# Kernel optimization log

Measured on AMD Instinct MI355X. Metric: run time of the kernel, lower is better.

The kernel has to match this reference:

```python
import jax, jax.numpy as jnp
import numpy as np

N0, N1, N2 = 100000, 20000, 4000   # nodes per hierarchy level
F, H, C = 128, 128, 10             # num_features, hidden_dim, num_classes
E0, E1, E2 = 1600000, 320000, 64000  # intra-level edges (avg degree 16)
EPS = 1e-5                          # BatchNorm eps


def setup_inputs() -> dict:
    key = jax.random.key(0)
    ks = jax.random.split(key, 16)
    s = 0.05
    return {
        "x": jax.random.normal(ks[0], (N0, F), jnp.float32),
        "ei0": jax.random.randint(ks[1], (2, E0), 0, N0),
        "ei1": jax.random.randint(ks[2], (2, E1), 0, N1),
        "ei2": jax.random.randint(ks[3], (2, E2), 0, N2),
        "parent1": jax.random.randint(ks[4], (N0,), 0, N1),
        "parent2": jax.random.randint(ks[5], (N1,), 0, N2),
        "W0": jax.random.normal(ks[6], (F, H), jnp.float32) * s,
        "b0": jnp.zeros((H,), jnp.float32),
        "W1": jax.random.normal(ks[7], (H, H), jnp.float32) * s,
        "b1": jnp.zeros((H,), jnp.float32),
        "W2": jax.random.normal(ks[8], (H, H), jnp.float32) * s,
        "b2": jnp.zeros((H,), jnp.float32),
        "W3": jax.random.normal(ks[9], (2 * H, H), jnp.float32) * s,
        "b3": jnp.zeros((H,), jnp.float32),
        "W4": jax.random.normal(ks[10], (2 * H, C), jnp.float32) * s,
        "b4": jnp.zeros((C,), jnp.float32),
        "pW": jax.random.normal(ks[11], (4, H, H), jnp.float32) * s,
        "pb": jnp.zeros((4, H), jnp.float32),
        "pgamma": jnp.ones((4, H), jnp.float32),
        "pbeta": jnp.zeros((4, H), jnp.float32),
        "pmean": jax.random.normal(ks[12], (4, H), jnp.float32) * 0.1,
        "pvar": jax.random.uniform(ks[13], (4, H), jnp.float32, 0.5, 1.5),
    }


def _gcn(x, ei, W, b):
    # GCNConv: add self loops, symmetric D^-1/2 (A+I) D^-1/2 normalization.
    n = x.shape[0]
    loops = jnp.arange(n)
    row = jnp.concatenate([ei[0], loops])  # source nodes
    col = jnp.concatenate([ei[1], loops])  # target nodes
    deg = jax.ops.segment_sum(jnp.ones(row.shape, x.dtype), col, num_segments=n)
    dis = deg ** -0.5  # deg >= 1 because of self loops
    norm = dis[row] * dis[col]
    xw = x @ W
    out = jax.ops.segment_sum(norm[:, None] * xw[row], col, num_segments=n)
    return out + b


def _pool_nn(y, W, b, g, beta, mean, var):
    # SEPooling nn: Linear -> ReLU -> BatchNorm1d (eval mode, running stats)
    y = jax.nn.relu(y @ W + b)
    return (y - mean) * (g / jnp.sqrt(var + EPS)) + beta


def reference(x, ei0, ei1, ei2, parent1, parent2,
              W0, b0, W1, b1, W2, b2, W3, b3, W4, b4,
              pW, pb, pgamma, pbeta, pmean, pvar):
    relu = jax.nn.relu
    # down path (dropout is identity in eval mode)
    h0 = relu(_gcn(x, ei0, W0, b0))  # [N0,H]; stored skip xs[0]
    p = jax.ops.segment_sum(h0, parent1, num_segments=N1)  # scatter-add children -> parents
    x1 = relu(_pool_nn(p, pW[0], pb[0], pgamma[0], pbeta[0], pmean[0], pvar[0]))
    h1 = relu(_gcn(x1, ei1, W1, b1))  # [N1,H]; stored skip xs[1]
    p = jax.ops.segment_sum(h1, parent2, num_segments=N2)
    x2 = relu(_pool_nn(p, pW[1], pb[1], pgamma[1], pbeta[1], pmean[1], pvar[1]))
    # up path: conv, unpool (gather parent feature per child), concat skip
    h = relu(_gcn(x2, ei2, W2, b2))  # [N2,H]
    xu = relu(_pool_nn(h[parent2], pW[2], pb[2], pgamma[2], pbeta[2], pmean[2], pvar[2]))  # [N1,H]
    xc = jnp.concatenate([xu, h1], axis=1)  # [N1,2H]
    h = relu(_gcn(xc, ei1, W3, b3))  # [N1,H]
    xu = relu(_pool_nn(h[parent1], pW[3], pb[3], pgamma[3], pbeta[3], pmean[3], pvar[3]))  # [N0,H]
    xc = jnp.concatenate([xu, h0], axis=1)  # [N0,2H]
    out = _gcn(xc, ei0, W4, b4)  # [N0,C]
    return jax.nn.log_softmax(out, axis=-1)
```

## Files before the change

kernel.cpp:

```cpp
#include <hip/hip_runtime.h>
#include <math.h>

#define N0 100000
#define N1 20000
#define N2 4000
#define HDIM 128
#define E0C 1600000
#define E1C 320000
#define E2C 64000
#define EPSBN 1e-5f

typedef unsigned int u32;
typedef float f32x4 __attribute__((ext_vector_type(4)));
typedef short bf16x8 __attribute__((ext_vector_type(8)));

union FragU { uint4 u; bf16x8 h; };
__device__ __forceinline__ bf16x8 asbf(uint4 v) { FragU x; x.u = v; return x.h; }

__device__ __forceinline__ float bl(u32 p) { return __uint_as_float(p << 16); }
__device__ __forceinline__ float bh(u32 p) { return __uint_as_float(p & 0xFFFF0000u); }
__device__ __forceinline__ u32 pack2(float a, float b) {
    u32 ua = __float_as_uint(a), ub = __float_as_uint(b);
    ua = (ua + 0x7FFFu + ((ua >> 16) & 1u)) >> 16;
    ub = (ub + 0x7FFFu + ((ub >> 16) & 1u)) >> 16;
    return ua | (ub << 16);
}

#define OFF0 0
#define OFF1 (N0)
#define OFF2 (N0 + N1)
#define OFF3 (N0 + N1 + N2)
#define OFF4 (N0 + N1 + N2 + N1)
#define OFFT (N0 + N1 + N2 + N1 + N2)

#define S0 (E0C)
#define S1 (E0C + E1C)
#define S2 (E0C + E1C + E2C)
#define S3 (E0C + E1C + E2C + N0)
#define S4 (E0C + E1C + E2C + N0 + N1)

#define NBUCK ((OFFT + 1023) / 1024)
#define ITEMS_PER_BLK 2048
#define NBA ((S4 + ITEMS_PER_BLK - 1) / ITEMS_PER_BLK)
#define BH_N (NBUCK * NBA)
#define NBLK2 ((BH_N + 1023) / 1024)

#define NWMAT 9


__device__ __forceinline__ void item_full(int g,
    const int* __restrict__ ei0r, const int* __restrict__ ei0c,
    const int* __restrict__ ei1r, const int* __restrict__ ei1c,
    const int* __restrict__ ei2r, const int* __restrict__ ei2c,
    const int* __restrict__ p1, const int* __restrict__ p2,
    int& concat, int& payload)
{
    if (g < S0)      { concat = ei0c[g];             payload = ei0r[g]; }
    else if (g < S1) { int i = g - S0; concat = OFF1 + ei1c[i]; payload = ei1r[i]; }
    else if (g < S2) { int i = g - S1; concat = OFF2 + ei2c[i]; payload = ei2r[i]; }
    else if (g < S3) { int i = g - S2; concat = OFF3 + p1[i];   payload = i; }
    else             { int i = g - S3; concat = OFF4 + p2[i];   payload = i; }
}

__device__ __forceinline__ int item_concat(int g,
    const int* __restrict__ ei0c, const int* __restrict__ ei1c, const int* __restrict__ ei2c,
    const int* __restrict__ p1, const int* __restrict__ p2)
{
    if (g < S0)      return ei0c[g];
    else if (g < S1) return OFF1 + ei1c[g - S0];
    else if (g < S2) return OFF2 + ei2c[g - S1];
    else if (g < S3) return OFF3 + p1[g - S2];
    else             return OFF4 + p2[g - S3];
}

__global__ __launch_bounds__(256) void binhist_kernel(
    const int* __restrict__ ei0c, const int* __restrict__ ei1c, const int* __restrict__ ei2c,
    const int* __restrict__ p1, const int* __restrict__ p2,
    int* __restrict__ blockHist,
    const float* __restrict__ W0p, const float* __restrict__ W1p,
    const float* __restrict__ W2p, const float* __restrict__ W3p,
    const float* __restrict__ pWp, u32* __restrict__ Wpk)
{
    __shared__ int hist[NBUCK];
    int tid = threadIdx.x, blk = blockIdx.x;
    if (blk >= NBA) {
        int b = blk - NBA;
        const float* src;
        if (b == 0) src = W0p;
        else if (b == 1) src = W1p;
        else if (b == 2) src = W2p;
        else if (b == 3) src = W3p;
        else if (b == 4) src = W3p + 128 * 128;
        else src = pWp + (b - 5) * 128 * 128;
        u32* dst = Wpk + b * 8192;
        #pragma unroll
        for (int it = 0; it < 32; it++) {
            int flat = it * 256 + tid;
            int i = flat & 3;
            int ln = (flat >> 2) & 63;
            int s = (flat >> 8) & 3;
            int t = flat >> 10;
            int mm = ln & 15, qq = ln >> 4;
            int k0 = s * 32 + qq * 8 + 2 * i;
            int col = t * 16 + mm;
            dst[flat] = pack2(src[k0 * 128 + col], src[(k0 + 1) * 128 + col]);
        }
        return;
    }
    for (int i = tid; i < NBUCK; i += 256) hist[i] = 0;
    __syncthreads();
    int base = blk * ITEMS_PER_BLK;
    #pragma unroll
    for (int k = 0; k < ITEMS_PER_BLK / 256; k++) {
        int g = base + k * 256 + tid;
        if (g < S4) {
            int c = item_concat(g, ei0c, ei1c, ei2c, p1, p2);
            atomicAdd(&hist[c >> 10], 1);
        }
    }
    __syncthreads();
    for (int b = tid; b < NBUCK; b += 256) blockHist[b * NBA + blk] = hist[b];
}

__global__ __launch_bounds__(256) void scan_k1(const int* __restrict__ c, int* __restrict__ bsum, int n) {
    int t = threadIdx.x;
    int base = blockIdx.x * 1024 + t * 4;
    int s = 0;
    #pragma unroll
    for (int j = 0; j < 4; j++) {
        int idx = base + j;
        if (idx < n) s += c[idx];
    }
    #pragma unroll
    for (int o = 32; o > 0; o >>= 1) s += __shfl_down(s, o, 64);
    __shared__ int ws[4];
    if ((t & 63) == 0) ws[t >> 6] = s;
    __syncthreads();
    if (t == 0) bsum[blockIdx.x] = ws[0] + ws[1] + ws[2] + ws[3];
}

__global__ __launch_bounds__(256) void scan_k2(int* __restrict__ bsum, int* __restrict__ totalOut, int nb,
    const float* __restrict__ g, const float* __restrict__ beta,
    const float* __restrict__ mean, const float* __restrict__ var,
    float* __restrict__ scale, float* __restrict__ shift)
{
    int t = threadIdx.x;
    #pragma unroll
    for (int j = 0; j < 2; j++) {
        int i = j * 256 + t;
        float s = g[i] * rsqrtf(var[i] + EPSBN);
        scale[i] = s;
        shift[i] = beta[i] - mean[i] * s;
    }
    int v = (t < nb) ? bsum[t] : 0;
    __shared__ int ts[256];
    ts[t] = v;
    __syncthreads();
    for (int o = 1; o < 256; o <<= 1) {
        int u = (t >= o) ? ts[t - o] : 0;
        __syncthreads();
        ts[t] += u;
        __syncthreads();
    }
    if (t < nb) bsum[t] = ts[t] - v;
    if (t == nb - 1) *totalOut = ts[t];
}

__global__ __launch_bounds__(256) void scan_k3(const int* __restrict__ c, const int* __restrict__ bsum,
                                               const int* __restrict__ total,
                                               int* __restrict__ S, int n) {
    int t = threadIdx.x;
    int base = blockIdx.x * 1024 + t * 4;
    int v[4];
    #pragma unroll
    for (int j = 0; j < 4; j++) v[j] = (base + j < n) ? c[base + j] : 0;
    int tsum = v[0] + v[1] + v[2] + v[3];
    __shared__ int ts[256];
    ts[t] = tsum;
    __syncthreads();
    for (int o = 1; o < 256; o <<= 1) {
        int u = (t >= o) ? ts[t - o] : 0;
        __syncthreads();
        ts[t] += u;
        __syncthreads();
    }
    int run = bsum[blockIdx.x] + ts[t] - tsum;
    #pragma unroll
    for (int j = 0; j < 4; j++) {
        if (base + j < n) { S[base + j] = run; run += v[j]; }
    }
    if (blockIdx.x == 0 && t == 0) S[n] = *total;
}

__global__ __launch_bounds__(256) void binfill_kernel(
    const int* __restrict__ ei0r, const int* __restrict__ ei0c,
    const int* __restrict__ ei1r, const int* __restrict__ ei1c,
    const int* __restrict__ ei2r, const int* __restrict__ ei2c,
    const int* __restrict__ p1, const int* __restrict__ p2,
    const int* __restrict__ OfsAbs, u32* __restrict__ binPair)
{
    __shared__ int cur[NBUCK];
    int tid = threadIdx.x, blk = blockIdx.x;
    for (int i = tid; i < NBUCK; i += 256) cur[i] = OfsAbs[i * NBA + blk];
    __syncthreads();
    int base = blk * ITEMS_PER_BLK;
    #pragma unroll
    for (int k = 0; k < ITEMS_PER_BLK / 256; k++) {
        int g = base + k * 256 + tid;
        if (g < S4) {
            int c, p;
            item_full(g, ei0r, ei0c, ei1r, ei1c, ei2r, ei2c, p1, p2, c, p);
            int pos = atomicAdd(&cur[c >> 10], 1);
            binPair[pos] = ((u32)(c & 1023) << 17) | (u32)p;
        }
    }
}

__global__ __launch_bounds__(1024) void bucket_build_kernel(
    const u32* __restrict__ binPair, const int* __restrict__ OfsAbs,
    int* __restrict__ rpAll, int* __restrict__ srcU,
    float* __restrict__ dis0, float* __restrict__ dis1, float* __restrict__ dis2)
{
    __shared__ int cnt_l[1024];
    __shared__ int rp_l[1024];
    __shared__ int ts2[1024];
    int b = blockIdx.x, tid = threadIdx.x;
    int start = OfsAbs[b * NBA];
    int end = (b + 1 < NBUCK) ? OfsAbs[(b + 1) * NBA] : S4;
    int d0 = b << 10;
    int nd = OFFT - d0; if (nd > 1024) nd = 1024;

    cnt_l[tid] = 0;
    __syncthreads();
    for (int i = start + tid; i < end; i += 1024) {
        u32 e = binPair[i];
        atomicAdd(&cnt_l[e >> 17], 1);
    }
    __syncthreads();
    int v = cnt_l[tid];
    ts2[tid] = v;
    __syncthreads();
    for (int o = 1; o < 1024; o <<= 1) {
        int u = (tid >= o) ? ts2[tid - o] : 0;
        __syncthreads();
        ts2[tid] += u;
        __syncthreads();
    }
    rp_l[tid] = ts2[tid] - v;
    __syncthreads();
    if (tid < nd) {
        int g = d0 + tid;
        rpAll[g] = start + rp_l[tid];
        float dv = rsqrtf((float)(v + 1));
        if (g < OFF1) dis0[g] = dv;
        else if (g < OFF2) dis1[g - OFF1] = dv;
        else if (g < OFF3) dis2[g - OFF2] = dv;
    }
    if (b == NBUCK - 1 && tid == 0) rpAll[OFFT] = S4;
    __syncthreads();
    for (int i = start + tid; i < end; i += 1024) {
        u32 e = binPair[i];
        int pos = start + atomicAdd(&rp_l[e >> 17], 1);
        srcU[pos] = (int)(e & 0x1FFFFu);
    }
}


#define G128_LOAD(sym, off) u32 sym = y[(long long)srcl[e + off] * 64 + lane]

__global__ __launch_bounds__(256) void gather128_kernel(
    const int* __restrict__ rp, const int* __restrict__ srcl,
    const u32* __restrict__ y, const float* __restrict__ dis,
    const float* __restrict__ bias, u32* __restrict__ h, int n)
{
    int wid = (int)((blockIdx.x * 256 + threadIdx.x) >> 6);
    int lane = threadIdx.x & 63;
    if (wid >= n) return;
    u32 self = y[(long long)wid * 64 + lane];
    float ax = bl(self), ay = bh(self);
    int e = rp[wid], e1 = rp[wid + 1];
    for (; e + 7 < e1; e += 8) {
        G128_LOAD(p0, 0); G128_LOAD(p1, 1); G128_LOAD(p2, 2); G128_LOAD(p3, 3);
        G128_LOAD(p4, 4); G128_LOAD(p5, 5); G128_LOAD(p6, 6); G128_LOAD(p7, 7);
        ax += ((bl(p0) + bl(p1)) + (bl(p2) + bl(p3))) + ((bl(p4) + bl(p5)) + (bl(p6) + bl(p7)));
        ay += ((bh(p0) + bh(p1)) + (bh(p2) + bh(p3))) + ((bh(p4) + bh(p5)) + (bh(p6) + bh(p7)));
    }
    if (e + 3 < e1) {
        G128_LOAD(p0, 0); G128_LOAD(p1, 1); G128_LOAD(p2, 2); G128_LOAD(p3, 3);
        ax += (bl(p0) + bl(p1)) + (bl(p2) + bl(p3));
        ay += (bh(p0) + bh(p1)) + (bh(p2) + bh(p3));
        e += 4;
    }
    if (e + 1 < e1) {
        G128_LOAD(p0, 0); G128_LOAD(p1, 1);
        ax += bl(p0) + bl(p1);
        ay += bh(p0) + bh(p1);
        e += 2;
    }
    if (e < e1) {
        G128_LOAD(p0, 0);
        ax += bl(p0); ay += bh(p0);
    }
    float d = dis[wid];
    float2 b = ((const float2*)bias)[lane];
    float r0 = fmaxf(fmaf(d, ax, b.x), 0.f);
    float r1 = fmaxf(fmaf(d, ay, b.y), 0.f);
    h[(long long)wid * 64 + lane] = pack2(r0, r1);
}

__global__ __launch_bounds__(256) void gather10_lsm_kernel(
    const int* __restrict__ rp, const int* __restrict__ srcl,
    const u32* __restrict__ y4, const float* __restrict__ dis,
    const float* __restrict__ bias, float* __restrict__ out, int n)
{
    int c = blockIdx.x * blockDim.x + threadIdx.x;
    if (c >= n) return;
    float acc[10];
    {
        long long base = (long long)c * 8;
        uint4 q = *(const uint4*)(y4 + base);
        u32 q4 = y4[base + 4];
        acc[0] = bl(q.x); acc[1] = bh(q.x);
        acc[2] = bl(q.y); acc[3] = bh(q.y);
        acc[4] = bl(q.z); acc[5] = bh(q.z);
        acc[6] = bl(q.w); acc[7] = bh(q.w);
        acc[8] = bl(q4);  acc[9] = bh(q4);
    }
    int e = rp[c], e1 = rp[c + 1];
    for (; e + 3 < e1; e += 4) {
        long long bA = (long long)srcl[e] * 8;
        long long bB = (long long)srcl[e + 1] * 8;
        long long bC = (long long)srcl[e + 2] * 8;
        long long bD = (long long)srcl[e + 3] * 8;
        uint4 qa = *(const uint4*)(y4 + bA); u32 qa4 = y4[bA + 4];
        uint4 qb = *(const uint4*)(y4 + bB); u32 qb4 = y4[bB + 4];
        uint4 qc = *(const uint4*)(y4 + bC); u32 qc4 = y4[bC + 4];
        uint4 qd = *(const uint4*)(y4 + bD); u32 qd4 = y4[bD + 4];
        acc[0] += (bl(qa.x) + bl(qb.x)) + (bl(qc.x) + bl(qd.x));
        acc[1] += (bh(qa.x) + bh(qb.x)) + (bh(qc.x) + bh(qd.x));
        acc[2] += (bl(qa.y) + bl(qb.y)) + (bl(qc.y) + bl(qd.y));
        acc[3] += (bh(qa.y) + bh(qb.y)) + (bh(qc.y) + bh(qd.y));
        acc[4] += (bl(qa.z) + bl(qb.z)) + (bl(qc.z) + bl(qd.z));
        acc[5] += (bh(qa.z) + bh(qb.z)) + (bh(qc.z) + bh(qd.z));
        acc[6] += (bl(qa.w) + bl(qb.w)) + (bl(qc.w) + bl(qd.w));
        acc[7] += (bh(qa.w) + bh(qb.w)) + (bh(qc.w) + bh(qd.w));
        acc[8] += (bl(qa4) + bl(qb4)) + (bl(qc4) + bl(qd4));
        acc[9] += (bh(qa4) + bh(qb4)) + (bh(qc4) + bh(qd4));
    }
    for (; e < e1; e++) {
        long long bA = (long long)srcl[e] * 8;
        uint4 qa = *(const uint4*)(y4 + bA);
        u32 qa4 = y4[bA + 4];
        acc[0] += bl(qa.x); acc[1] += bh(qa.x);
        acc[2] += bl(qa.y); acc[3] += bh(qa.y);
        acc[4] += bl(qa.z); acc[5] += bh(qa.z);
        acc[6] += bl(qa.w); acc[7] += bh(qa.w);
        acc[8] += bl(qa4);  acc[9] += bh(qa4);
    }
    float d = dis[c];
    float m = -1e30f;
    #pragma unroll
    for (int k = 0; k < 10; k++) {
        acc[k] = fmaf(d, acc[k], bias[k]);
        m = fmaxf(m, acc[k]);
    }
    float s = 0.f;
    #pragma unroll
    for (int k = 0; k < 10; k++) s += expf(acc[k] - m);
    float ls = logf(s);
    #pragma unroll
    for (int k = 0; k < 10; k++) out[(long long)c * 10 + k] = acc[k] - m - ls;
}

__global__ __launch_bounds__(256) void mm128_kernel(
    const void* __restrict__ Av, const u32* __restrict__ Wp,
    u32* __restrict__ out, int M,
    const float* __restrict__ dis,
    const u32* __restrict__ gsrc, const int* __restrict__ gidx,
    const float* __restrict__ bias,
    const float* __restrict__ bnscale, const float* __restrict__ bnshift,
    int pool, int afp32,
    const int* __restrict__ pp, const int* __restrict__ childl, int apool)
{
    __shared__ u32 WL[8192];
    int tid = threadIdx.x;
    {
        const uint4* ws4 = (const uint4*)Wp;
        uint4* wd4 = (uint4*)WL;
        #pragma unroll
        for (int it = 0; it < 8; it++) wd4[it * 256 + tid] = ws4[it * 256 + tid];
    }
    __syncthreads();

    int lane = tid & 63;
    int w = tid >> 6;
    int m = lane & 15, q = lane >> 4;
    int row = blockIdx.x * 64 + w * 16 + m;
    bool live = (row < M);

    uint4 xb[4];
    if (live) {
        if (apool) {
            float fa[32];
            #pragma unroll
            for (int i = 0; i < 32; i++) fa[i] = 0.f;
            const u32* Hb = (const u32*)Av;
            int e = pp[row], eE = pp[row + 1];
            for (; e < eE; e++) {
                long long cb = (long long)childl[e] * 64;
                #pragma unroll
                for (int s = 0; s < 4; s++) {
                    uint4 vv = *(const uint4*)(Hb + cb + s * 16 + q * 4);
                    fa[s * 8 + 0] += bl(vv.x); fa[s * 8 + 1] += bh(vv.x);
                    fa[s * 8 + 2] += bl(vv.y); fa[s * 8 + 3] += bh(vv.y);
                    fa[s * 8 + 4] += bl(vv.z); fa[s * 8 + 5] += bh(vv.z);
                    fa[s * 8 + 6] += bl(vv.w); fa[s * 8 + 7] += bh(vv.w);
                }
            }
            #pragma unroll
            for (int s = 0; s < 4; s++) {
                xb[s].x = pack2(fa[s * 8 + 0], fa[s * 8 + 1]);
                xb[s].y = pack2(fa[s * 8 + 2], fa[s * 8 + 3]);
                xb[s].z = pack2(fa[s * 8 + 4], fa[s * 8 + 5]);
                xb[s].w = pack2(fa[s * 8 + 6], fa[s * 8 + 7]);
            }
        } else if (afp32) {
            const float* Af = (const float*)Av;
            #pragma unroll
            for (int s = 0; s < 4; s++) {
                const float4* p = (const float4*)(Af + (long long)row * 128 + s * 32 + q * 8);
                float4 f0 = p[0], f1 = p[1];
                xb[s].x = pack2(f0.x, f0.y);
                xb[s].y = pack2(f0.z, f0.w);
                xb[s].z = pack2(f1.x, f1.y);
                xb[s].w = pack2(f1.z, f1.w);
            }
        } else {
            const u32* Ab = (const u32*)Av;
            #pragma unroll
            for (int s = 0; s < 4; s++)
                xb[s] = *(const uint4*)(Ab + (long long)row * 64 + s * 16 + q * 4);
        }
    } else {
        xb[0] = xb[1] = xb[2] = xb[3] = make_uint4(0u, 0u, 0u, 0u);
    }

    float d = 1.0f;
    if (dis && live) d = dis[row];
    long long gbase = (gsrc && live) ? (long long)gidx[row] * 64 : 0;

    #pragma unroll
    for (int t = 0; t < 8; t++) {
        f32x4 acc = {0.f, 0.f, 0.f, 0.f};
        #pragma unroll
        for (int s = 0; s < 4; s++) {
            uint4 wa = *(const uint4*)&WL[((t * 4 + s) * 64 + lane) * 4];
            acc = __builtin_amdgcn_mfma_f32_16x16x32_bf16(asbf(wa), asbf(xb[s]), acc, 0, 0, 0);
        }
        if (live) {
            float v0 = acc[0], v1 = acc[1], v2 = acc[2], v3 = acc[3];
            int cbase = t * 16 + q * 4;
            if (gsrc) {
                uint2 g = *(const uint2*)(gsrc + gbase + (cbase >> 1));
                v0 += bl(g.x); v1 += bh(g.x);
                v2 += bl(g.y); v3 += bh(g.y);
            }
            if (pool) {
                float4 bb = *(const float4*)(bias + cbase);
                float4 sc = *(const float4*)(bnscale + cbase);
                float4 sh = *(const float4*)(bnshift + cbase);
                v0 = fmaxf(fmaxf(v0 + bb.x, 0.f) * sc.x + sh.x, 0.f);
                v1 = fmaxf(fmaxf(v1 + bb.y, 0.f) * sc.y + sh.y, 0.f);
                v2 = fmaxf(fmaxf(v2 + bb.z, 0.f) * sc.z + sh.z, 0.f);
                v3 = fmaxf(fmaxf(v3 + bb.w, 0.f) * sc.w + sh.w, 0.f);
            }
            v0 *= d; v1 *= d; v2 *= d; v3 *= d;
            uint2 st;
            st.x = pack2(v0, v1);
            st.y = pack2(v2, v3);
            *(uint2*)(out + (long long)row * 64 + (cbase >> 1)) = st;
        }
    }
}

#define TLP 68
__global__ __launch_bounds__(256) void mm128x2_kernel(
    const u32* __restrict__ Av, const u32* __restrict__ Wa, const u32* __restrict__ Wb,
    u32* __restrict__ out, int M,
    const float* __restrict__ dis2,
    const float* __restrict__ bias1,
    const float* __restrict__ bnscale1, const float* __restrict__ bnshift1,
    const int* __restrict__ pp, const int* __restrict__ childl, int apool)
{
    __shared__ u32 WL[8192];
    __shared__ u32 TL[64 * TLP];
    int tid = threadIdx.x;
    {
        const uint4* ws4 = (const uint4*)Wa;
        uint4* wd4 = (uint4*)WL;
        #pragma unroll
        for (int it = 0; it < 8; it++) wd4[it * 256 + tid] = ws4[it * 256 + tid];
    }
    __syncthreads();

    int lane = tid & 63;
    int w = tid >> 6;
    int m = lane & 15, q = lane >> 4;
    int row = blockIdx.x * 64 + w * 16 + m;
    bool live = (row < M);

    uint4 xb[4];
    if (live) {
        if (apool) {
            float fa[32];
            #pragma unroll
            for (int i = 0; i < 32; i++) fa[i] = 0.f;
            int e = pp[row], eE = pp[row + 1];
            for (; e < eE; e++) {
                long long cb = (long long)childl[e] * 64;
                #pragma unroll
                for (int s = 0; s < 4; s++) {
                    uint4 vv = *(const uint4*)(Av + cb + s * 16 + q * 4);
                    fa[s * 8 + 0] += bl(vv.x); fa[s * 8 + 1] += bh(vv.x);
                    fa[s * 8 + 2] += bl(vv.y); fa[s * 8 + 3] += bh(vv.y);
                    fa[s * 8 + 4] += bl(vv.z); fa[s * 8 + 5] += bh(vv.z);
                    fa[s * 8 + 6] += bl(vv.w); fa[s * 8 + 7] += bh(vv.w);
                }
            }
            #pragma unroll
            for (int s = 0; s < 4; s++) {
                xb[s].x = pack2(fa[s * 8 + 0], fa[s * 8 + 1]);
                xb[s].y = pack2(fa[s * 8 + 2], fa[s * 8 + 3]);
                xb[s].z = pack2(fa[s * 8 + 4], fa[s * 8 + 5]);
                xb[s].w = pack2(fa[s * 8 + 6], fa[s * 8 + 7]);
            }
        } else {
            #pragma unroll
            for (int s = 0; s < 4; s++)
                xb[s] = *(const uint4*)(Av + (long long)row * 64 + s * 16 + q * 4);
        }
    } else {
        xb[0] = xb[1] = xb[2] = xb[3] = make_uint4(0u, 0u, 0u, 0u);
    }

    u32* tl = TL + (w * 16 + m) * TLP;

    #pragma unroll
    for (int t = 0; t < 8; t++) {
        f32x4 acc = {0.f, 0.f, 0.f, 0.f};
        #pragma unroll
        for (int s = 0; s < 4; s++) {
            uint4 wa4 = *(const uint4*)&WL[((t * 4 + s) * 64 + lane) * 4];
            acc = __builtin_amdgcn_mfma_f32_16x16x32_bf16(asbf(wa4), asbf(xb[s]), acc, 0, 0, 0);
        }
        int cbase = t * 16 + q * 4;
        float4 bb = *(const float4*)(bias1 + cbase);
        float4 sc = *(const float4*)(bnscale1 + cbase);
        float4 sh = *(const float4*)(bnshift1 + cbase);
        float v0 = fmaxf(fmaxf(acc[0] + bb.x, 0.f) * sc.x + sh.x, 0.f);
        float v1 = fmaxf(fmaxf(acc[1] + bb.y, 0.f) * sc.y + sh.y, 0.f);
        float v2 = fmaxf(fmaxf(acc[2] + bb.z, 0.f) * sc.z + sh.z, 0.f);
        float v3 = fmaxf(fmaxf(acc[3] + bb.w, 0.f) * sc.w + sh.w, 0.f);
        uint2 st;
        st.x = pack2(v0, v1);
        st.y = pack2(v2, v3);
        *(uint2*)&tl[t * 8 + q * 2] = st;
    }
    __syncthreads();
    {
        const uint4* ws4 = (const uint4*)Wb;
        uint4* wd4 = (uint4*)WL;
        #pragma unroll
        for (int it = 0; it < 8; it++) wd4[it * 256 + tid] = ws4[it * 256 + tid];
    }
    __syncthreads();

    #pragma unroll
    for (int s = 0; s < 4; s++)
        xb[s] = *(const uint4*)&tl[s * 16 + q * 4];
    float d = 1.0f;
    if (dis2 && live) d = dis2[row];

    #pragma unroll
    for (int t = 0; t < 8; t++) {
        f32x4 acc = {0.f, 0.f, 0.f, 0.f};
        #pragma unroll
        for (int s = 0; s < 4; s++) {
            uint4 wa4 = *(const uint4*)&WL[((t * 4 + s) * 64 + lane) * 4];
            acc = __builtin_amdgcn_mfma_f32_16x16x32_bf16(asbf(wa4), asbf(xb[s]), acc, 0, 0, 0);
        }
        if (live) {
            int cbase = t * 16 + q * 4;
            float v0 = acc[0] * d, v1 = acc[1] * d, v2 = acc[2] * d, v3 = acc[3] * d;
            uint2 st;
            st.x = pack2(v0, v1);
            st.y = pack2(v2, v3);
            *(uint2*)(out + (long long)row * 64 + (cbase >> 1)) = st;
        }
    }
}

__global__ __launch_bounds__(256) void mm10_kernel(
    const u32* __restrict__ A, const float* __restrict__ W,
    float* __restrict__ out, int M)
{
    __shared__ float Ws[128 * 10];
    for (int i = threadIdx.x; i < 1280; i += 256) Ws[i] = W[i];
    __syncthreads();
    int row = blockIdx.x * blockDim.x + threadIdx.x;
    if (row >= M) return;
    const uint4* a = (const uint4*)(A + (long long)row * 64);
    float acc[10] = {0, 0, 0, 0, 0, 0, 0, 0, 0, 0};
    #pragma unroll 4
    for (int i = 0; i < 16; i++) {
        uint4 av = a[i];
        int k = i * 8;
        float f[8] = { bl(av.x), bh(av.x), bl(av.y), bh(av.y),
                       bl(av.z), bh(av.z), bl(av.w), bh(av.w) };
        #pragma unroll
        for (int j = 0; j < 8; j++) {
            #pragma unroll
            for (int cc = 0; cc < 10; cc++)
                acc[cc] += f[j] * Ws[(k + j) * 10 + cc];
        }
    }
    #pragma unroll
    for (int cc = 0; cc < 10; cc++) out[(long long)row * 10 + cc] = acc[cc];
}

__global__ __launch_bounds__(256) void mm10p_kernel(
    const u32* __restrict__ A, const float* __restrict__ W,
    u32* __restrict__ outp, int M,
    const float* __restrict__ dis,
    const float* __restrict__ gsrc, const int* __restrict__ gidx)
{
    __shared__ float Ws[128 * 10];
    for (int i = threadIdx.x; i < 1280; i += 256) Ws[i] = W[i];
    __syncthreads();
    int row = blockIdx.x * blockDim.x + threadIdx.x;
    if (row >= M) return;
    const uint4* a = (const uint4*)(A + (long long)row * 64);
    float acc[10] = {0, 0, 0, 0, 0, 0, 0, 0, 0, 0};
    #pragma unroll 4
    for (int i = 0; i < 16; i++) {
        uint4 av = a[i];
        int k = i * 8;
        float f[8] = { bl(av.x), bh(av.x), bl(av.y), bh(av.y),
                       bl(av.z), bh(av.z), bl(av.w), bh(av.w) };
        #pragma unroll
        for (int j = 0; j < 8; j++) {
            #pragma unroll
            for (int cc = 0; cc < 10; cc++)
                acc[cc] += f[j] * Ws[(k + j) * 10 + cc];
        }
    }
    float d = dis[row];
    const float* g = gsrc + (long long)gidx[row] * 10;
    long long base = (long long)row * 8;
    #pragma unroll
    for (int j = 0; j < 5; j++) {
        float v0 = (acc[2 * j] + g[2 * j]) * d;
        float v1 = (acc[2 * j + 1] + g[2 * j + 1]) * d;
        outp[base + j] = pack2(v0, v1);
    }
}


extern "C" void kernel_launch(void* const* d_in, const int* in_sizes, int n_in,
                              void* d_out, int out_size, void* d_ws, size_t ws_size,
                              hipStream_t stream) {
    const float* x       = (const float*)d_in[0];
    const int*   ei0     = (const int*)d_in[1];
    const int*   ei1     = (const int*)d_in[2];
    const int*   ei2     = (const int*)d_in[3];
    const int*   parent1 = (const int*)d_in[4];
    const int*   parent2 = (const int*)d_in[5];
    const float* W0 = (const float*)d_in[6];
    const float* b0 = (const float*)d_in[7];
    const float* W1 = (const float*)d_in[8];
    const float* b1 = (const float*)d_in[9];
    const float* W2 = (const float*)d_in[10];
    const float* b2 = (const float*)d_in[11];
    const float* W3 = (const float*)d_in[12];
    const float* b3 = (const float*)d_in[13];
    const float* W4 = (const float*)d_in[14];
    const float* b4 = (const float*)d_in[15];
    const float* pW = (const float*)d_in[16];
    const float* pb = (const float*)d_in[17];
    const float* pg = (const float*)d_in[18];
    const float* pbeta = (const float*)d_in[19];
    const float* pmean = (const float*)d_in[20];
    const float* pvar  = (const float*)d_in[21];
    float* out = (float*)d_out;

    char* ws = (char*)d_ws;
    size_t off = 0;
    auto alloc = [&](size_t nbytes) -> char* {
        char* p = ws + off;
        off += ((nbytes + 255) / 256) * 256;
        return p;
    };
    float* dis0 = (float*)alloc(N0 * 4);
    float* dis1 = (float*)alloc(N1 * 4);
    float* dis2 = (float*)alloc(N2 * 4);
    float* bnscale = (float*)alloc(4 * HDIM * 4);
    float* bnshift = (float*)alloc(4 * HDIM * 4);
    float* W1b = (float*)alloc((size_t)N1 * 10 * 4);
    u32* Y   = (u32*)alloc((size_t)N0 * 64 * 4);
    u32* H0  = (u32*)alloc((size_t)N0 * 64 * 4);
    u32* H1  = (u32*)alloc((size_t)N1 * 64 * 4);
    u32* HU1 = (u32*)alloc((size_t)N1 * 64 * 4);
    u32* U1  = (u32*)alloc((size_t)N1 * 64 * 4);
    u32* H2  = (u32*)alloc((size_t)N2 * 64 * 4);
    u32* V2  = (u32*)alloc((size_t)N2 * 64 * 4);
    u32* Y4p = (u32*)alloc((size_t)N0 * 8 * 4);
    u32* Wpk = (u32*)alloc((size_t)NWMAT * 8192 * 4);
    int* rpAll = (int*)alloc((size_t)(OFFT + 1) * 4);
    int* srcU  = (int*)alloc((size_t)S4 * 4);
    int* blockHist = (int*)alloc((size_t)BH_N * 4);
    int* OfsAbs    = (int*)alloc((size_t)(BH_N + 1) * 4);
    u32* binPair   = (u32*)alloc((size_t)S4 * 4);
    int* bsum   = (int*)alloc(NBLK2 * 4);
    int* totalb = (int*)alloc(4);

    const int B = 256;
    auto G = [](long long t) { return (unsigned)((t + 255) / 256); };
    auto G64 = [](long long m) { return (unsigned)((m + 63) / 64); };

    binhist_kernel<<<NBA + NWMAT, B, 0, stream>>>(
        ei0 + E0C, ei1 + E1C, ei2 + E2C, parent1, parent2, blockHist,
        W0, W1, W2, W3, pW, Wpk);
    scan_k1<<<NBLK2, B, 0, stream>>>(blockHist, bsum, BH_N);
    scan_k2<<<1, B, 0, stream>>>(bsum, totalb, NBLK2, pg, pbeta, pmean, pvar, bnscale, bnshift);
    scan_k3<<<NBLK2, B, 0, stream>>>(blockHist, bsum, totalb, OfsAbs, BH_N);
    binfill_kernel<<<NBA, B, 0, stream>>>(
        ei0, ei0 + E0C, ei1, ei1 + E1C, ei2, ei2 + E2C, parent1, parent2, OfsAbs, binPair);
    bucket_build_kernel<<<NBUCK, 1024, 0, stream>>>(
        binPair, OfsAbs, rpAll, srcU, dis0, dis1, dis2);

    mm128_kernel<<<G64(N0), B, 0, stream>>>(
        x, Wpk + 0 * 8192, Y, N0, dis0, nullptr, nullptr, nullptr, nullptr, nullptr, 0, 1,
        nullptr, nullptr, 0);
    gather128_kernel<<<G((long long)N0 * 64), B, 0, stream>>>(rpAll + OFF0, srcU, Y, dis0, b0, H0, N0);

    mm128x2_kernel<<<G64(N1), B, 0, stream>>>(
        H0, Wpk + 5 * 8192, Wpk + 1 * 8192, Y, N1, dis1,
        pb, bnscale, bnshift, rpAll + OFF3, srcU, 1);
    gather128_kernel<<<G((long long)N1 * 64), B, 0, stream>>>(rpAll + OFF1, srcU, Y, dis1, b1, H1, N1);

    mm128x2_kernel<<<G64(N2), B, 0, stream>>>(
        H1, Wpk + 6 * 8192, Wpk + 2 * 8192, Y, N2, dis2,
        pb + 128, bnscale + 128, bnshift + 128, rpAll + OFF4, srcU, 1);
    gather128_kernel<<<G((long long)N2 * 64), B, 0, stream>>>(rpAll + OFF2, srcU, Y, dis2, b2, H2, N2);

    mm128x2_kernel<<<G64(N2), B, 0, stream>>>(
        H2, Wpk + 7 * 8192, Wpk + 3 * 8192, V2, N2, nullptr,
        pb + 256, bnscale + 256, bnshift + 256, nullptr, nullptr, 0);

    mm128_kernel<<<G64(N1), B, 0, stream>>>(
        H1, Wpk + 4 * 8192, Y, N1, dis1, V2, parent2, nullptr, nullptr, nullptr, 0, 0,
        nullptr, nullptr, 0);
    gather128_kernel<<<G((long long)N1 * 64), B, 0, stream>>>(rpAll + OFF1, srcU, Y, dis1, b3, HU1, N1);

    mm128_kernel<<<G64(N1), B, 0, stream>>>(
        HU1, Wpk + 8 * 8192, U1, N1, nullptr, nullptr, nullptr, pb + 384, bnscale + 384, bnshift + 384, 1, 0,
        nullptr, nullptr, 0);
    mm10_kernel<<<G(N1), B, 0, stream>>>(U1, W4, W1b, N1);

    mm10p_kernel<<<G(N0), B, 0, stream>>>(H0, W4 + 128 * 10, Y4p, N0, dis0, W1b, parent1);
    gather10_lsm_kernel<<<G(N0), B, 0, stream>>>(rpAll + OFF0, srcU, Y4p, dis0, b4, out, N0);
}
```

Measured before the change: 392.4 us.

## Store level-0 GEMM output in column slices for cache-friendly GCN gather

The first 128-wide GEMM now writes its output in 8 column slices of 16 features (slice-major layout) instead of row-major. A new gather kernel assigns each block to one slice, so the random neighbour gathers for the 100k-node level touch a table about one eighth the size, which is meant to fit better in L2/LLC. The cost is shorter 32-byte accesses per neighbour row, eight times more index reads of the edge list, and an extra slice-aware store path in the GEMM kernel.

```diff
diff --git a/kernel.cpp b/kernel.cpp
--- a/kernel.cpp
+++ b/kernel.cpp
@@ -308,6 +308,48 @@
     h[(long long)wid * 64 + lane] = pack2(r0, r1);
 }
 
+__global__ __launch_bounds__(256) void gather128s_kernel(
+    const int* __restrict__ rp, const int* __restrict__ srcl,
+    const u32* __restrict__ ys, const float* __restrict__ dis,
+    const float* __restrict__ bias, u32* __restrict__ h, int n)
+{
+    int blk = blockIdx.x;
+    int s = blk & 7;
+    int chunk = blk >> 3;
+    int tid = threadIdx.x;
+    int w = tid >> 6, lane = tid & 63;
+    int rloc = lane >> 3;
+    int lane8 = lane & 7;
+    int r = chunk * 32 + w * 8 + rloc;
+    if (r >= n) return;
+    const u32* Y = ys + (long long)s * n * 8;
+    u32 self = Y[(long long)r * 8 + lane8];
+    float ax = bl(self), ay = bh(self);
+    int e = rp[r], e1 = rp[r + 1];
+    for (; e + 3 < e1; e += 4) {
+        int i0 = __builtin_nontemporal_load(srcl + e);
+        int i1 = __builtin_nontemporal_load(srcl + e + 1);
+        int i2 = __builtin_nontemporal_load(srcl + e + 2);
+        int i3 = __builtin_nontemporal_load(srcl + e + 3);
+        u32 p0 = Y[(long long)i0 * 8 + lane8];
+        u32 p1 = Y[(long long)i1 * 8 + lane8];
+        u32 p2 = Y[(long long)i2 * 8 + lane8];
+        u32 p3 = Y[(long long)i3 * 8 + lane8];
+        ax += (bl(p0) + bl(p1)) + (bl(p2) + bl(p3));
+        ay += (bh(p0) + bh(p1)) + (bh(p2) + bh(p3));
+    }
+    for (; e < e1; e++) {
+        int i0 = __builtin_nontemporal_load(srcl + e);
+        u32 p0 = Y[(long long)i0 * 8 + lane8];
+        ax += bl(p0); ay += bh(p0);
+    }
+    float d = dis[r];
+    float2 b = ((const float2*)bias)[s * 8 + lane8];
+    float r0 = fmaxf(fmaf(d, ax, b.x), 0.f);
+    float r1 = fmaxf(fmaf(d, ay, b.y), 0.f);
+    h[(long long)r * 64 + s * 8 + lane8] = pack2(r0, r1);
+}
+
 __global__ __launch_bounds__(256) void gather10_lsm_kernel(
     const int* __restrict__ rp, const int* __restrict__ srcl,
     const u32* __restrict__ y4, const float* __restrict__ dis,
@@ -380,7 +422,8 @@
     const float* __restrict__ bias,
     const float* __restrict__ bnscale, const float* __restrict__ bnshift,
     int pool, int afp32,
-    const int* __restrict__ pp, const int* __restrict__ childl, int apool)
+    const int* __restrict__ pp, const int* __restrict__ childl, int apool,
+    int sliceout)
 {
     __shared__ u32 WL[8192];
     int tid = threadIdx.x;
@@ -478,7 +521,10 @@
             uint2 st;
             st.x = pack2(v0, v1);
             st.y = pack2(v2, v3);
-            *(uint2*)(out + (long long)row * 64 + (cbase >> 1)) = st;
+            if (sliceout)
+                *(uint2*)(out + ((long long)t * M + row) * 8 + q * 2) = st;
+            else
+                *(uint2*)(out + (long long)row * 64 + (cbase >> 1)) = st;
         }
     }
 }
@@ -740,8 +786,9 @@
 
     mm128_kernel<<<G64(N0), B, 0, stream>>>(
         x, Wpk + 0 * 8192, Y, N0, dis0, nullptr, nullptr, nullptr, nullptr, nullptr, 0, 1,
-        nullptr, nullptr, 0);
-    gather128_kernel<<<G((long long)N0 * 64), B, 0, stream>>>(rpAll + OFF0, srcU, Y, dis0, b0, H0, N0);
+        nullptr, nullptr, 0, 1);
+    gather128s_kernel<<<((N0 + 31) / 32) * 8, B, 0, stream>>>(
+        rpAll + OFF0, srcU, Y, dis0, b0, H0, N0);
 
     mm128x2_kernel<<<G64(N1), B, 0, stream>>>(
         H0, Wpk + 5 * 8192, Wpk + 1 * 8192, Y, N1, dis1,
@@ -759,12 +806,12 @@
 
     mm128_kernel<<<G64(N1), B, 0, stream>>>(
         H1, Wpk + 4 * 8192, Y, N1, dis1, V2, parent2, nullptr, nullptr, nullptr, 0, 0,
-        nullptr, nullptr, 0);
+        nullptr, nullptr, 0, 0);
     gather128_kernel<<<G((long long)N1 * 64), B, 0, stream>>>(rpAll + OFF1, srcU, Y, dis1, b3, HU1, N1);
 
     mm128_kernel<<<G64(N1), B, 0, stream>>>(
         HU1, Wpk + 8 * 8192, U1, N1, nullptr, nullptr, nullptr, pb + 384, bnscale + 384, bnshift + 384, 1, 0,
-        nullptr, nullptr, 0);
+        nullptr, nullptr, 0, 0);
     mm10_kernel<<<G(N1), B, 0, stream>>>(U1, W4, W1b, N1);
 
     mm10p_kernel<<<G(N0), B, 0, stream>>>(H0, W4 + 128 * 10, Y4p, N0, dis0, W1b, parent1);
```

After: 515.8 us. +31.5%, slower.

## Fuse pool MLP and 10-class projection; use wave-shuffle scan in bucket build

Applied to the files above, without the earlier changes.

The bucket build kernel's 1024-element Hillis-Steele shared-memory scan, which needs a barrier at every step, is replaced with a wave-level shuffle scan plus a small cross-wave pass, cutting down on barriers. The separate N1 pool MLP (mm128) and the 10-column projection (mm10) are merged into one kernel. It keeps the bf16 MLP output tile in LDS and multiplies by W4 there, so the U1 intermediate is no longer written to and read back from global memory and one launch disappears. The fused kernel uses more LDS per block, which may lower occupancy, and the small matmul runs from LDS with a strided 640-slot loop.

```diff
diff --git a/kernel.cpp b/kernel.cpp
--- a/kernel.cpp
+++ b/kernel.cpp
@@ -223,7 +223,7 @@
 {
     __shared__ int cnt_l[1024];
     __shared__ int rp_l[1024];
-    __shared__ int ts2[1024];
+    __shared__ int wsum[16];
     int b = blockIdx.x, tid = threadIdx.x;
     int start = OfsAbs[b * NBA];
     int end = (b + 1 < NBUCK) ? OfsAbs[(b + 1) * NBA] : S4;
@@ -238,15 +238,27 @@
     }
     __syncthreads();
     int v = cnt_l[tid];
-    ts2[tid] = v;
-    __syncthreads();
-    for (int o = 1; o < 1024; o <<= 1) {
-        int u = (tid >= o) ? ts2[tid - o] : 0;
-        __syncthreads();
-        ts2[tid] += u;
-        __syncthreads();
-    }
-    rp_l[tid] = ts2[tid] - v;
+    int lane = tid & 63, wv = tid >> 6;
+    int s = v;
+    #pragma unroll
+    for (int o = 1; o < 64; o <<= 1) {
+        int u = __shfl_up(s, o, 64);
+        if (lane >= o) s += u;
+    }
+    if (lane == 63) wsum[wv] = s;
+    __syncthreads();
+    if (wv == 0) {
+        int t2 = (lane < 16) ? wsum[lane] : 0;
+        #pragma unroll
+        for (int o = 1; o < 16; o <<= 1) {
+            int u = __shfl_up(t2, o, 64);
+            if (lane >= o) t2 += u;
+        }
+        if (lane < 16) wsum[lane] = t2;
+    }
+    __syncthreads();
+    int incl = s + (wv ? wsum[wv - 1] : 0);
+    rp_l[tid] = incl - v;
     __syncthreads();
     if (tid < nd) {
         int g = d0 + tid;
@@ -600,32 +612,81 @@
     }
 }
 
-__global__ __launch_bounds__(256) void mm10_kernel(
-    const u32* __restrict__ A, const float* __restrict__ W,
-    float* __restrict__ out, int M)
-{
+__global__ __launch_bounds__(256) void mm128_mm10_kernel(
+    const u32* __restrict__ Av, const u32* __restrict__ Wp,
+    const float* __restrict__ W10,
+    float* __restrict__ out10, int M,
+    const float* __restrict__ bias1,
+    const float* __restrict__ bnscale1, const float* __restrict__ bnshift1)
+{
+    __shared__ u32 WL[8192];
+    __shared__ u32 TL[64 * TLP];
     __shared__ float Ws[128 * 10];
-    for (int i = threadIdx.x; i < 1280; i += 256) Ws[i] = W[i];
-    __syncthreads();
-    int row = blockIdx.x * blockDim.x + threadIdx.x;
-    if (row >= M) return;
-    const uint4* a = (const uint4*)(A + (long long)row * 64);
-    float acc[10] = {0, 0, 0, 0, 0, 0, 0, 0, 0, 0};
-    #pragma unroll 4
-    for (int i = 0; i < 16; i++) {
-        uint4 av = a[i];
-        int k = i * 8;
-        float f[8] = { bl(av.x), bh(av.x), bl(av.y), bh(av.y),
-                       bl(av.z), bh(av.z), bl(av.w), bh(av.w) };
-        #pragma unroll
-        for (int j = 0; j < 8; j++) {
+    int tid = threadIdx.x;
+    {
+        const uint4* ws4 = (const uint4*)Wp;
+        uint4* wd4 = (uint4*)WL;
+        #pragma unroll
+        for (int it = 0; it < 8; it++) wd4[it * 256 + tid] = ws4[it * 256 + tid];
+    }
+    for (int i = tid; i < 1280; i += 256) Ws[i] = W10[i];
+    __syncthreads();
+
+    int lane = tid & 63;
+    int w = tid >> 6;
+    int m = lane & 15, q = lane >> 4;
+    int row = blockIdx.x * 64 + w * 16 + m;
+    bool live = (row < M);
+
+    uint4 xb[4];
+    if (live) {
+        #pragma unroll
+        for (int s = 0; s < 4; s++)
+            xb[s] = *(const uint4*)(Av + (long long)row * 64 + s * 16 + q * 4);
+    } else {
+        xb[0] = xb[1] = xb[2] = xb[3] = make_uint4(0u, 0u, 0u, 0u);
+    }
+
+    u32* tl = TL + (w * 16 + m) * TLP;
+
+    #pragma unroll
+    for (int t = 0; t < 8; t++) {
+        f32x4 acc = {0.f, 0.f, 0.f, 0.f};
+        #pragma unroll
+        for (int s = 0; s < 4; s++) {
+            uint4 wa4 = *(const uint4*)&WL[((t * 4 + s) * 64 + lane) * 4];
+            acc = __builtin_amdgcn_mfma_f32_16x16x32_bf16(asbf(wa4), asbf(xb[s]), acc, 0, 0, 0);
+        }
+        int cbase = t * 16 + q * 4;
+        float4 bb = *(const float4*)(bias1 + cbase);
+        float4 sc = *(const float4*)(bnscale1 + cbase);
+        float4 sh = *(const float4*)(bnshift1 + cbase);
+        float v0 = fmaxf(fmaxf(acc[0] + bb.x, 0.f) * sc.x + sh.x, 0.f);
+        float v1 = fmaxf(fmaxf(acc[1] + bb.y, 0.f) * sc.y + sh.y, 0.f);
+        float v2 = fmaxf(fmaxf(acc[2] + bb.z, 0.f) * sc.z + sh.z, 0.f);
+        float v3 = fmaxf(fmaxf(acc[3] + bb.w, 0.f) * sc.w + sh.w, 0.f);
+        uint2 st;
+        st.x = pack2(v0, v1);
+        st.y = pack2(v2, v3);
+        *(uint2*)&tl[t * 8 + q * 2] = st;
+    }
+    __syncthreads();
+
+    int base = blockIdx.x * 64;
+    for (int slot = tid; slot < 640; slot += 256) {
+        int r = slot / 10, cc = slot % 10;
+        if (base + r < M) {
+            const u32* tr = &TL[r * TLP];
+            float acc = 0.f;
             #pragma unroll
-            for (int cc = 0; cc < 10; cc++)
-                acc[cc] += f[j] * Ws[(k + j) * 10 + cc];
-        }
-    }
-    #pragma unroll
-    for (int cc = 0; cc < 10; cc++) out[(long long)row * 10 + cc] = acc[cc];
+            for (int k2 = 0; k2 < 64; k2++) {
+                u32 p = tr[k2];
+                acc += bl(p) * Ws[(2 * k2) * 10 + cc];
+                acc += bh(p) * Ws[(2 * k2 + 1) * 10 + cc];
+            }
+            out10[(long long)(base + r) * 10 + cc] = acc;
+        }
+    }
 }
 
 __global__ __launch_bounds__(256) void mm10p_kernel(
@@ -710,7 +771,6 @@
     u32* H0  = (u32*)alloc((size_t)N0 * 64 * 4);
     u32* H1  = (u32*)alloc((size_t)N1 * 64 * 4);
     u32* HU1 = (u32*)alloc((size_t)N1 * 64 * 4);
-    u32* U1  = (u32*)alloc((size_t)N1 * 64 * 4);
     u32* H2  = (u32*)alloc((size_t)N2 * 64 * 4);
     u32* V2  = (u32*)alloc((size_t)N2 * 64 * 4);
     u32* Y4p = (u32*)alloc((size_t)N0 * 8 * 4);
@@ -762,10 +822,8 @@
         nullptr, nullptr, 0);
     gather128_kernel<<<G((long long)N1 * 64), B, 0, stream>>>(rpAll + OFF1, srcU, Y, dis1, b3, HU1, N1);
 
-    mm128_kernel<<<G64(N1), B, 0, stream>>>(
-        HU1, Wpk + 8 * 8192, U1, N1, nullptr, nullptr, nullptr, pb + 384, bnscale + 384, bnshift + 384, 1, 0,
-        nullptr, nullptr, 0);
-    mm10_kernel<<<G(N1), B, 0, stream>>>(U1, W4, W1b, N1);
+    mm128_mm10_kernel<<<G64(N1), B, 0, stream>>>(
+        HU1, Wpk + 8 * 8192, W4, W1b, N1, pb + 384, bnscale + 384, bnshift + 384);
 
     mm10p_kernel<<<G(N0), B, 0, stream>>>(H0, W4 + 128 * 10, Y4p, N0, dis0, W1b, parent1);
     gather10_lsm_kernel<<<G(N0), B, 0, stream>>>(rpAll + OFF0, srcU, Y4p, dis0, b4, out, N0);
```

Result: no change. 385.6 us (-1.7%).
